# Kernel tuning notes

Hardware: AMD Instinct MI355X
Metric: run time of the kernel (lower is better)

The kernel has to match this reference:

```python
import jax, jax.numpy as jnp
import numpy as np

B, N_DET, N_T, NY, NX = 4, 128, 2048, 256, 256


def setup_inputs() -> dict:
    key = jax.random.key(0)
    k1, k2, k3 = jax.random.split(key, 3)
    sino = jax.random.normal(k1, (B, 1, N_DET, N_T), dtype=jnp.float32)
    # LUT channel 0: floor temporal index (stored as float, cast to int in forward)
    k_floor = jax.random.randint(k2, (NY, NX, N_DET), 0, N_T).astype(jnp.float32)
    # LUT channel 1: linear interpolation weight alpha in [0,1)
    alpha = jax.random.uniform(k3, (NY, NX, N_DET), dtype=jnp.float32)
    lut = jnp.stack([k_floor, alpha], axis=-1)  # [NY, NX, N_DET, 2]
    return {"sino": sino, "lut": lut}


def reference(sino, lut):
    # sino: [B, 1, n_det, n_t]; lut: [ny, nx, n_det, 2]
    b, c, n_det, n_t = sino.shape
    k_floor = lut[..., 0].astype(jnp.int32)          # [ny, nx, n_det]
    alpha = lut[..., 1]                               # [ny, nx, n_det]
    valid = (k_floor >= 0) & (k_floor < n_t - 1)
    k0 = jnp.clip(k_floor, 0, n_t - 2)
    k1 = k0 + 1
    S = sino[:, 0]                                    # [B, n_det, n_t]
    det = jnp.arange(n_det)                           # broadcasts against [ny,nx,n_det]
    s0 = S[:, det, k0]                                # [B, ny, nx, n_det]
    s1 = S[:, det, k1]                                # [B, ny, nx, n_det]
    sk = (1.0 - alpha) * s0 + alpha * s1
    sk = jnp.where(valid, sk, jnp.zeros_like(sk))
    # Hann apodization window over detectors
    apod = (0.5 - 0.5 * jnp.cos(2.0 * jnp.pi * jnp.arange(n_det, dtype=jnp.float32)
                                / max(n_det - 1, 1))).astype(sino.dtype)
    out = jnp.einsum('bijd,d->bij', sk, apod)
    norm = jnp.maximum(apod.sum(), 1e-06)
    out = out / norm
    return out[:, None]                               # [B, 1, ny, nx]
```

## Files before the change

### kernel.cpp

```cpp
#include <hip/hip_runtime.h>
#include <hip/hip_fp16.h>


#define NB      4
#define NDET    128
#define NT      2048
#define NPIX    65536
#define DBLOCK  8
#define DPH     4
#define NPHASE  4
#define PTILE   1024
#define THREADS 512
#define PXPT    (PTILE / THREADS)

__global__ __launch_bounds__(THREADS, 4)
void bp_kernel(const float* __restrict__ sino,
               const float* __restrict__ lut,
               float* __restrict__ out) {
    __shared__ __half2 lds[DPH][NT];

    const int tid   = threadIdx.x;
    const int octet = blockIdx.x & 15;
    const int tile  = blockIdx.x >> 4;
    const int d0    = octet * DBLOCK;
    const int px0   = tile * PTILE;

    float apod[DBLOCK];
#pragma unroll
    for (int j = 0; j < DBLOCK; ++j) {
        float x = (float)(d0 + j) * (6.28318530717958647692f / 127.0f);
        apod[j] = 0.5f - 0.5f * __cosf(x);
    }

    float4 L[PXPT][4];
#pragma unroll
    for (int i = 0; i < PXPT; ++i) {
        const float4* lp = (const float4*)
            (lut + ((size_t)(px0 + tid + i * THREADS) * NDET + d0) * 2);
#pragma unroll
        for (int q = 0; q < 4; ++q) L[i][q] = lp[q];
    }

    float acc[PXPT][NB];
#pragma unroll
    for (int i = 0; i < PXPT; ++i)
#pragma unroll
        for (int b = 0; b < NB; ++b) acc[i][b] = 0.0f;

    const float4* s4 = (const float4*)sino;

    for (int ph = 0; ph < NPHASE; ++ph) {
        const int bp  = ph >> 1;
        const int dh  = ph & 1;
        const int b0  = bp * 2;
        const int dg0 = d0 + dh * DPH;
        if (ph) __syncthreads();

        for (int f = tid; f < DPH * (NT / 4); f += THREADS) {
            int dl = f >> 9;
            int t4 = f & 511;
            size_t row = ((size_t)b0 * NDET + dg0 + dl) * (NT / 4) + t4;
            float4 ve = s4[row];
            float4 vo = s4[row + (size_t)NDET * (NT / 4)];
            __half2* dst = &lds[dl][t4 * 4];
            dst[0] = __floats2half2_rn(ve.x, vo.x);
            dst[1] = __floats2half2_rn(ve.y, vo.y);
            dst[2] = __floats2half2_rn(ve.z, vo.z);
            dst[3] = __floats2half2_rn(ve.w, vo.w);
        }
        __syncthreads();

#pragma unroll
        for (int i = 0; i < PXPT; ++i) {
#pragma unroll
            for (int q2 = 0; q2 < 2; ++q2) {
                float4 Lq = L[i][dh * 2 + q2];
#pragma unroll
                for (int h = 0; h < 2; ++h) {
                    float kf = h ? Lq.z : Lq.x;
                    float af = h ? Lq.w : Lq.y;
                    int   dl = q2 * 2 + h;
                    int k = (int)kf;
                    bool valid = (unsigned)k < (unsigned)(NT - 1);
                    float w  = valid ? apod[dh * DPH + dl] : 0.0f;
                    int  k0  = valid ? k : 0;
                    __half2 s0v = lds[dl][k0];
                    __half2 s1v = lds[dl][k0 + 1];
                    __half2 a2  = __float2half2_rn(af);
                    __half2 sk  = __hfma2(a2, __hsub2(s1v, s0v), s0v);
                    float2  fv  = __half22float2(sk);
                    acc[i][b0 + 0] = fmaf(w, fv.x, acc[i][b0 + 0]);
                    acc[i][b0 + 1] = fmaf(w, fv.y, acc[i][b0 + 1]);
                }
            }
        }
    }

    const float inv_norm = 1.0f / 63.5f;
#pragma unroll
    for (int i = 0; i < PXPT; ++i) {
        const int px = px0 + tid + i * THREADS;
#pragma unroll
        for (int b = 0; b < NB; ++b) {
            atomicAdd(&out[(size_t)b * NPIX + px], acc[i][b] * inv_norm);
        }
    }
}

extern "C" void kernel_launch(void* const* d_in, const int* in_sizes, int n_in,
                              void* d_out, int out_size, void* d_ws, size_t ws_size,
                              hipStream_t stream) {
    const float* sino = (const float*)d_in[0];
    const float* lut  = (const float*)d_in[1];
    float* out = (float*)d_out;

    (void)hipMemsetAsync(d_out, 0, (size_t)out_size * sizeof(float), stream);

    bp_kernel<<<dim3(1024), dim3(THREADS), 0, stream>>>(sino, lut, out);
}
```

Measured before the change: 127.1 us.

## Pre-convert sinogram to packed fp16 batch-interleaved workspace before backprojection

A separate conversion kernel first writes the sinogram as fp16 with all four batches packed into one 8-byte element per (detector, time) sample, stored in a workspace buffer. The main kernel then copies this packed data straight into LDS and does one pair of LDS reads per detector that serves all four batches, where before it needed a separate read per batch pair. This removes the per-block fp32-to-fp16 conversion and halves the number of LUT-indexed LDS gathers. The cost is an extra kernel launch and a round trip through global memory for the workspace, plus a fallback path that is used when the workspace is too small.

```diff
diff --git a/kernel.cpp b/kernel.cpp
--- a/kernel.cpp
+++ b/kernel.cpp
@@ -7,17 +7,32 @@
 #define NT      2048
 #define NPIX    65536
 #define DBLOCK  8
-#define DPH     4
+#define DPH     2
 #define NPHASE  4
 #define PTILE   1024
 #define THREADS 512
 #define PXPT    (PTILE / THREADS)
 
+__global__ __launch_bounds__(256)
+void cvt_kernel(const float* __restrict__ sino, uint2* __restrict__ ws16) {
+    const int id = blockIdx.x * 256 + threadIdx.x;
+    float v0 = sino[id];
+    float v1 = sino[id + NDET * NT];
+    float v2 = sino[id + 2 * NDET * NT];
+    float v3 = sino[id + 3 * NDET * NT];
+    __half2 h01 = __floats2half2_rn(v0, v1);
+    __half2 h23 = __floats2half2_rn(v2, v3);
+    uint2 u;
+    u.x = *(const unsigned*)&h01;
+    u.y = *(const unsigned*)&h23;
+    ws16[id] = u;
+}
+
 __global__ __launch_bounds__(THREADS, 4)
-void bp_kernel(const float* __restrict__ sino,
+void bp_kernel(const uint2* __restrict__ ws16,
                const float* __restrict__ lut,
                float* __restrict__ out) {
-    __shared__ __half2 lds[DPH][NT];
+    __shared__ uint2 lds2[DPH * NT];
 
     const int tid   = threadIdx.x;
     const int octet = blockIdx.x & 15;
@@ -32,44 +47,120 @@
         apod[j] = 0.5f - 0.5f * __cosf(x);
     }
 
-    float4 L[PXPT][4];
+    float4 L[PXPT][NPHASE];
 #pragma unroll
     for (int i = 0; i < PXPT; ++i) {
         const float4* lp = (const float4*)
             (lut + ((size_t)(px0 + tid + i * THREADS) * NDET + d0) * 2);
 #pragma unroll
+        for (int q = 0; q < NPHASE; ++q) L[i][q] = lp[q];
+    }
+
+    float acc[PXPT][NB];
+#pragma unroll
+    for (int i = 0; i < PXPT; ++i)
+#pragma unroll
+        for (int b = 0; b < NB; ++b) acc[i][b] = 0.0f;
+
+    for (int ph = 0; ph < NPHASE; ++ph) {
+        const int dg0 = d0 + ph * DPH;
+        if (ph) __syncthreads();
+
+        {
+            const uint4* src = (const uint4*)(ws16 + (size_t)dg0 * NT);
+            uint4* dst = (uint4*)lds2;
+            for (int f = tid; f < DPH * NT / 2; f += THREADS)
+                dst[f] = src[f];
+        }
+        __syncthreads();
+
+#pragma unroll
+        for (int i = 0; i < PXPT; ++i) {
+            float4 Lq = L[i][ph];
+#pragma unroll
+            for (int h = 0; h < 2; ++h) {
+                float kf = h ? Lq.z : Lq.x;
+                float af = h ? Lq.w : Lq.y;
+                int k = (int)kf;
+                bool valid = (unsigned)k < (unsigned)(NT - 1);
+                float w  = valid ? apod[ph * DPH + h] : 0.0f;
+                int  k0  = valid ? k : 0;
+                uint2 e0 = lds2[h * NT + k0];
+                uint2 e1 = lds2[h * NT + k0 + 1];
+                __half2 a01 = *(__half2*)&e0.x, a23 = *(__half2*)&e0.y;
+                __half2 b01 = *(__half2*)&e1.x, b23 = *(__half2*)&e1.y;
+                __half2 a2  = __float2half2_rn(af);
+                __half2 s01 = __hfma2(a2, __hsub2(b01, a01), a01);
+                __half2 s23 = __hfma2(a2, __hsub2(b23, a23), a23);
+                float2 f01 = __half22float2(s01);
+                float2 f23 = __half22float2(s23);
+                acc[i][0] = fmaf(w, f01.x, acc[i][0]);
+                acc[i][1] = fmaf(w, f01.y, acc[i][1]);
+                acc[i][2] = fmaf(w, f23.x, acc[i][2]);
+                acc[i][3] = fmaf(w, f23.y, acc[i][3]);
+            }
+        }
+    }
+
+    const float inv_norm = 1.0f / 63.5f;
+#pragma unroll
+    for (int i = 0; i < PXPT; ++i) {
+        const int px = px0 + tid + i * THREADS;
+#pragma unroll
+        for (int b = 0; b < NB; ++b) {
+            atomicAdd(&out[(size_t)b * NPIX + px], acc[i][b] * inv_norm);
+        }
+    }
+}
+
+__global__ __launch_bounds__(THREADS, 4)
+void bp_fallback(const float* __restrict__ sino,
+                 const float* __restrict__ lut,
+                 float* __restrict__ out) {
+    __shared__ __half2 lds[4][NT];
+    const int tid   = threadIdx.x;
+    const int octet = blockIdx.x & 15;
+    const int tile  = blockIdx.x >> 4;
+    const int d0    = octet * DBLOCK;
+    const int px0   = tile * PTILE;
+    float apod[DBLOCK];
+#pragma unroll
+    for (int j = 0; j < DBLOCK; ++j) {
+        float x = (float)(d0 + j) * (6.28318530717958647692f / 127.0f);
+        apod[j] = 0.5f - 0.5f * __cosf(x);
+    }
+    float4 L[PXPT][4];
+#pragma unroll
+    for (int i = 0; i < PXPT; ++i) {
+        const float4* lp = (const float4*)
+            (lut + ((size_t)(px0 + tid + i * THREADS) * NDET + d0) * 2);
+#pragma unroll
         for (int q = 0; q < 4; ++q) L[i][q] = lp[q];
     }
-
     float acc[PXPT][NB];
 #pragma unroll
     for (int i = 0; i < PXPT; ++i)
 #pragma unroll
         for (int b = 0; b < NB; ++b) acc[i][b] = 0.0f;
-
     const float4* s4 = (const float4*)sino;
-
-    for (int ph = 0; ph < NPHASE; ++ph) {
-        const int bp  = ph >> 1;
+    for (int ph = 0; ph < 4; ++ph) {
+        const int b0  = (ph >> 1) * 2;
         const int dh  = ph & 1;
-        const int b0  = bp * 2;
-        const int dg0 = d0 + dh * DPH;
+        const int dg0 = d0 + dh * 4;
         if (ph) __syncthreads();
-
-        for (int f = tid; f < DPH * (NT / 4); f += THREADS) {
+        for (int f = tid; f < 4 * (NT / 4); f += THREADS) {
             int dl = f >> 9;
             int t4 = f & 511;
             size_t row = ((size_t)b0 * NDET + dg0 + dl) * (NT / 4) + t4;
             float4 ve = s4[row];
             float4 vo = s4[row + (size_t)NDET * (NT / 4)];
-            __half2* dst = &lds[dl][t4 * 4];
-            dst[0] = __floats2half2_rn(ve.x, vo.x);
-            dst[1] = __floats2half2_rn(ve.y, vo.y);
-            dst[2] = __floats2half2_rn(ve.z, vo.z);
-            dst[3] = __floats2half2_rn(ve.w, vo.w);
+            __half2* dstp = &lds[dl][t4 * 4];
+            dstp[0] = __floats2half2_rn(ve.x, vo.x);
+            dstp[1] = __floats2half2_rn(ve.y, vo.y);
+            dstp[2] = __floats2half2_rn(ve.z, vo.z);
+            dstp[3] = __floats2half2_rn(ve.w, vo.w);
         }
         __syncthreads();
-
 #pragma unroll
         for (int i = 0; i < PXPT; ++i) {
 #pragma unroll
@@ -82,7 +173,7 @@
                     int   dl = q2 * 2 + h;
                     int k = (int)kf;
                     bool valid = (unsigned)k < (unsigned)(NT - 1);
-                    float w  = valid ? apod[dh * DPH + dl] : 0.0f;
+                    float w  = valid ? apod[dh * 4 + dl] : 0.0f;
                     int  k0  = valid ? k : 0;
                     __half2 s0v = lds[dl][k0];
                     __half2 s1v = lds[dl][k0 + 1];
@@ -95,15 +186,13 @@
             }
         }
     }
-
     const float inv_norm = 1.0f / 63.5f;
 #pragma unroll
     for (int i = 0; i < PXPT; ++i) {
         const int px = px0 + tid + i * THREADS;
 #pragma unroll
-        for (int b = 0; b < NB; ++b) {
+        for (int b = 0; b < NB; ++b)
             atomicAdd(&out[(size_t)b * NPIX + px], acc[i][b] * inv_norm);
-        }
     }
 }
 
@@ -116,5 +205,12 @@
 
     (void)hipMemsetAsync(d_out, 0, (size_t)out_size * sizeof(float), stream);
 
-    bp_kernel<<<dim3(1024), dim3(THREADS), 0, stream>>>(sino, lut, out);
-}
+    const size_t ws_needed = (size_t)NDET * NT * sizeof(uint2);
+    if (ws_size >= ws_needed) {
+        uint2* ws16 = (uint2*)d_ws;
+        cvt_kernel<<<dim3(NDET * NT / 256), dim3(256), 0, stream>>>(sino, ws16);
+        bp_kernel<<<dim3(1024), dim3(THREADS), 0, stream>>>(ws16, lut, out);
+    } else {
+        bp_fallback<<<dim3(1024), dim3(THREADS), 0, stream>>>(sino, lut, out);
+    }
+}
```

After: 124.3 us. -2.2%, faster.
